# Optimization experiments

Measured on AMD Instinct MI355X. Metric: run time of the kernel, lower is better.

The kernel has to match this reference:

```python
import jax, jax.numpy as jnp
import numpy as np

B, T, C = 2, 2048, 1024
N_HEAD = 16
HEAD_DIM = C // N_HEAD


def setup_inputs() -> dict:
    key = jax.random.key(0)
    k1, k2, k3 = jax.random.split(key, 3)
    x = jax.random.normal(k1, (B, T, C), dtype=jnp.float32)
    # weights stored as [in, out]; torch Linear computes x @ W.T with weight [out, in]
    W_qkv = jax.random.normal(k2, (C, 3 * C), dtype=jnp.float32) * (1.0 / np.sqrt(C))
    W_proj = jax.random.normal(k3, (C, C), dtype=jnp.float32) * (1.0 / np.sqrt(C))
    return {"x": x, "W_qkv": W_qkv, "W_proj": W_proj}


def reference(x, W_qkv, W_proj):
    Bb, Tt, Cc = x.shape
    qkv = x @ W_qkv                                # [B,T,3C]
    q, k, v = jnp.split(qkv, 3, axis=2)
    # [B,T,H,D] -> [B,H,T,D]
    q = q.reshape(Bb, Tt, N_HEAD, HEAD_DIM).transpose(0, 2, 1, 3)
    k = k.reshape(Bb, Tt, N_HEAD, HEAD_DIM).transpose(0, 2, 1, 3)
    v = v.reshape(Bb, Tt, N_HEAD, HEAD_DIM).transpose(0, 2, 1, 3)
    scale = 1.0 / np.sqrt(HEAD_DIM).astype(np.float32)
    att = jnp.einsum('bhqd,bhkd->bhqk', q, k) * scale   # [B,H,T,T]
    causal = jnp.tril(jnp.ones((Tt, Tt), dtype=bool))
    att = jnp.where(causal[None, None], att, -jnp.inf)
    att = jax.nn.softmax(att, axis=-1)
    y = jnp.einsum('bhqk,bhkd->bhqd', att, v)           # [B,H,T,D]
    y = y.transpose(0, 2, 1, 3).reshape(Bb, Tt, Cc)
    return y @ W_proj
```

## Files before the change

kernel.cpp:

```cpp
#include <hip/hip_runtime.h>
#include <hip/hip_bf16.h>
#include <math.h>


typedef __bf16 bf16_t;
typedef __bf16 bf16x4 __attribute__((ext_vector_type(4)));
typedef __bf16 bf16x8 __attribute__((ext_vector_type(8)));
typedef float  f32x4  __attribute__((ext_vector_type(4)));

#define MFMA16(a, b, c) __builtin_amdgcn_mfma_f32_16x16x32_bf16((a), (b), (c), 0, 0, 0)

#define Bn 2
#define Tn 2048
#define Cn 1024
#define Hn 16
#define Dn 64
#define C3 3072
#define Mn 4096
#define QKW 2048
#define NEG_BIG (-1e30f)
#define SCL2 0.18033688011112042f
#define M2   17.31234049066756f

__device__ __forceinline__ void gload_lds16(const void* g, void* l) {
    __builtin_amdgcn_global_load_lds(
        (const __attribute__((address_space(1))) unsigned int*)g,
        (__attribute__((address_space(3))) unsigned int*)l, 16, 0, 0);
}

__global__ __launch_bounds__(256) void transpose_cvt(const float* __restrict__ in,
                                                     bf16_t* __restrict__ out,
                                                     int K, int N) {
    __shared__ float tile[32][33];
    int n0 = blockIdx.x * 32, k0 = blockIdx.y * 32;
    int tx = threadIdx.x, ty = threadIdx.y;
#pragma unroll
    for (int i = 0; i < 32; i += 8)
        tile[ty + i][tx] = in[(size_t)(k0 + ty + i) * N + n0 + tx];
    __syncthreads();
#pragma unroll
    for (int i = 0; i < 32; i += 8)
        out[(size_t)(n0 + ty + i) * K + k0 + tx] = (bf16_t)tile[tx][ty + i];
}

template <typename AT, typename CT, int MODE>
__global__ __launch_bounds__(256) void gemm_m97(const AT* __restrict__ A, int lda,
                                                const bf16_t* __restrict__ BT,
                                                CT* __restrict__ Cout, int ldc, int Kd,
                                                bf16_t* __restrict__ qk,
                                                bf16_t* __restrict__ vT) {
    constexpr bool AF32 = (sizeof(AT) == 4);
    __shared__ AT     As[128 * 32];
    __shared__ bf16_t Bs[128 * 32];

    const int tid = threadIdx.x;
    const int w = tid >> 6, lane = tid & 63;
    const int l16 = lane & 15, quad = lane >> 4;
    const int wm = w & 1, wn = w >> 1;
    const int n0 = blockIdx.x * 128;
    const int m0 = blockIdx.y * 128;

    f32x4 zero = {0.f, 0.f, 0.f, 0.f};
    f32x4 acc[4][4];
#pragma unroll
    for (int mb = 0; mb < 4; mb++)
#pragma unroll
        for (int nb = 0; nb < 4; nb++) acc[mb][nb] = zero;

    for (int k = 0; k < Kd; k += 32) {
        __syncthreads();
        if (AF32) {
#pragma unroll
            for (int j = 0; j < 4; j++) {
                int seg = w * 4 + j;
                int r = seg * 8 + (lane >> 3);
                int cc = (lane & 7) ^ (r & 7);
                const float* g = (const float*)A + (size_t)(m0 + r) * lda + k + cc * 4;
                gload_lds16(g, (char*)As + seg * 1024);
            }
        } else {
#pragma unroll
            for (int j = 0; j < 2; j++) {
                int seg = w * 2 + j;
                int r = seg * 16 + (lane >> 2);
                int cc = (lane & 3) ^ (r & 3);
                const bf16_t* g = (const bf16_t*)A + (size_t)(m0 + r) * lda + k + cc * 8;
                gload_lds16(g, (char*)As + seg * 1024);
            }
        }
#pragma unroll
        for (int j = 0; j < 2; j++) {
            int seg = w * 2 + j;
            int r = seg * 16 + (lane >> 2);
            int cc = (lane & 3) ^ (r & 3);
            const bf16_t* g = BT + (size_t)(n0 + r) * Kd + k + cc * 8;
            gload_lds16(g, (char*)Bs + seg * 1024);
        }
        __syncthreads();

        bf16x8 af[4], bf[4];
#pragma unroll
        for (int mb = 0; mb < 4; mb++) {
            int r = wm * 64 + mb * 16 + l16;
            if (AF32) {
                f32x4 x0 = *(const f32x4*)((const char*)As + (r * 8 + ((quad * 2) ^ (r & 7))) * 16);
                f32x4 x1 = *(const f32x4*)((const char*)As + (r * 8 + ((quad * 2 + 1) ^ (r & 7))) * 16);
                bf16x8 t;
                t[0] = (bf16_t)x0[0]; t[1] = (bf16_t)x0[1]; t[2] = (bf16_t)x0[2]; t[3] = (bf16_t)x0[3];
                t[4] = (bf16_t)x1[0]; t[5] = (bf16_t)x1[1]; t[6] = (bf16_t)x1[2]; t[7] = (bf16_t)x1[3];
                af[mb] = t;
            } else {
                af[mb] = *(const bf16x8*)((const char*)As + (r * 4 + (quad ^ (r & 3))) * 16);
            }
        }
#pragma unroll
        for (int nb = 0; nb < 4; nb++) {
            int r = wn * 64 + nb * 16 + l16;
            bf[nb] = *(const bf16x8*)((const char*)Bs + (r * 4 + (quad ^ (r & 3))) * 16);
        }
#pragma unroll
        for (int mb = 0; mb < 4; mb++)
#pragma unroll
            for (int nb = 0; nb < 4; nb++)
                acc[mb][nb] = MFMA16(af[mb], bf[nb], acc[mb][nb]);
    }

#pragma unroll
    for (int mb = 0; mb < 4; mb++)
#pragma unroll
        for (int nb = 0; nb < 4; nb++) {
            const int col = n0 + wn * 64 + nb * 16 + l16;
            const int row0 = m0 + wm * 64 + mb * 16 + quad * 4;
            if (MODE == 0) {
#pragma unroll
                for (int rr = 0; rr < 4; rr++)
                    Cout[(size_t)(row0 + rr) * ldc + col] = (CT)acc[mb][nb][rr];
            } else {
                if (col < 2048) {
#pragma unroll
                    for (int rr = 0; rr < 4; rr++)
                        qk[(size_t)(row0 + rr) * QKW + col] = (bf16_t)acc[mb][nb][rr];
                } else {
                    int hcol = col - 2048;
                    int bb = row0 >> 11, t0 = row0 & 2047;
                    bf16x4 pv;
#pragma unroll
                    for (int rr = 0; rr < 4; rr++) pv[rr] = (bf16_t)acc[mb][nb][rr];
                    *(bf16x4*)(vT + ((size_t)(bb * 1024 + hcol)) * Tn + t0) = pv;
                }
            }
        }
}

__global__ __launch_bounds__(256) void attn_kernel(bf16_t* __restrict__ qk,
                                                   const bf16_t* __restrict__ vT) {
    const int id = blockIdx.x;
    const int round = id >> 8;
    const int p = id & 255;
    const int bh = p & 31;
    const int xx = p >> 5;
    const int qt = round ? (15 - xx) : xx;
    const int b = bh >> 4, h = bh & 15;

    const int tid = threadIdx.x;
    const int wave = tid >> 6, lane = tid & 63;
    const int l16 = lane & 15, quad = lane >> 4;

    __shared__ bf16_t Kt[64][72];
    __shared__ bf16_t Vt[64][72];
    __shared__ bf16_t Pl[4][32][72];

    bf16_t* qbase = qk + (size_t)b * Tn * QKW + h * Dn;
    const bf16_t* kbase = qk + (size_t)b * Tn * QKW + Cn + h * Dn;
    const bf16_t* vbase = vT + (size_t)(b * 1024 + h * Dn) * Tn;

    const int q0 = qt * 128 + wave * 32;

    bf16x8 qf[2][2];
#pragma unroll
    for (int mb = 0; mb < 2; mb++)
#pragma unroll
        for (int ks = 0; ks < 2; ks++)
            qf[mb][ks] = *(const bf16x8*)(qbase + (size_t)(q0 + mb * 16 + l16) * QKW + ks * 32 + quad * 8);

    bf16x8 ones;
#pragma unroll
    for (int j = 0; j < 8; j++) ones[j] = (bf16_t)1.0f;

    f32x4 zero = {0.f, 0.f, 0.f, 0.f};
    f32x4 o[2][4];
    f32x4 ol[2];
#pragma unroll
    for (int mb = 0; mb < 2; mb++) {
#pragma unroll
        for (int i = 0; i < 4; i++) o[mb][i] = zero;
        ol[mb] = zero;
    }

    const int kbmax = 2 * qt + 1;
    const int kb_mask = 2 * qt + (wave >> 1);

    for (int kb = 0; kb <= kbmax; kb++) {
        __syncthreads();
        const int key0 = kb * 64;
        for (int c = tid; c < 512; c += 256) {
            int r = c >> 3, col = (c & 7) * 8;
            *(bf16x8*)(&Kt[r][col]) = *(const bf16x8*)(kbase + (size_t)(key0 + r) * QKW + col);
            *(bf16x8*)(&Vt[r][col]) = *(const bf16x8*)(vbase + (size_t)r * Tn + key0 + col);
        }
        __syncthreads();

        if (kb <= kb_mask) {
            f32x4 s[2][4];
#pragma unroll
            for (int mb = 0; mb < 2; mb++)
#pragma unroll
                for (int nbk = 0; nbk < 4; nbk++) s[mb][nbk] = zero;
#pragma unroll
            for (int nbk = 0; nbk < 4; nbk++) {
                bf16x8 kf0 = *(const bf16x8*)(&Kt[nbk * 16 + l16][quad * 8]);
                bf16x8 kf1 = *(const bf16x8*)(&Kt[nbk * 16 + l16][32 + quad * 8]);
#pragma unroll
                for (int mb = 0; mb < 2; mb++) {
                    s[mb][nbk] = MFMA16(kf0, qf[mb][0], s[mb][nbk]);
                    s[mb][nbk] = MFMA16(kf1, qf[mb][1], s[mb][nbk]);
                }
            }

            if (kb == kb_mask) {
#pragma unroll
                for (int nbk = 0; nbk < 4; nbk++) {
#pragma unroll
                    for (int mb = 0; mb < 2; mb++) {
                        int q = q0 + mb * 16 + l16;
#pragma unroll
                        for (int r = 0; r < 4; r++) {
                            int key = key0 + nbk * 16 + quad * 4 + r;
                            if (key > q) s[mb][nbk][r] = NEG_BIG;
                        }
                    }
                }
            }

#pragma unroll
            for (int mb = 0; mb < 2; mb++)
#pragma unroll
                for (int nbk = 0; nbk < 4; nbk++) {
                    bf16x4 pk;
#pragma unroll
                    for (int r = 0; r < 4; r++)
                        pk[r] = (bf16_t)__builtin_exp2f(__builtin_fmaf(s[mb][nbk][r], SCL2, -M2));
                    *(bf16x4*)(&Pl[wave][mb * 16 + l16][nbk * 16 + quad * 4]) = pk;
                }

#pragma unroll
            for (int ks = 0; ks < 2; ks++) {
                bf16x8 pf0 = *(const bf16x8*)(&Pl[wave][l16][ks * 32 + quad * 8]);
                bf16x8 pf1 = *(const bf16x8*)(&Pl[wave][16 + l16][ks * 32 + quad * 8]);
#pragma unroll
                for (int nbd = 0; nbd < 4; nbd++) {
                    bf16x8 vf = *(const bf16x8*)(&Vt[nbd * 16 + l16][ks * 32 + quad * 8]);
                    o[0][nbd] = MFMA16(pf0, vf, o[0][nbd]);
                    o[1][nbd] = MFMA16(pf1, vf, o[1][nbd]);
                }
                ol[0] = MFMA16(pf0, ones, ol[0]);
                ol[1] = MFMA16(pf1, ones, ol[1]);
            }
        }
    }

#pragma unroll
    for (int mb = 0; mb < 2; mb++)
#pragma unroll
        for (int nbd = 0; nbd < 4; nbd++)
#pragma unroll
            for (int r = 0; r < 4; r++) {
                int t = q0 + mb * 16 + quad * 4 + r;
                float val = o[mb][nbd][r] / ol[mb][r];
                qbase[(size_t)t * QKW + nbd * 16 + l16] = (bf16_t)val;
            }
}

extern "C" void kernel_launch(void* const* d_in, const int* in_sizes, int n_in,
                              void* d_out, int out_size, void* d_ws, size_t ws_size,
                              hipStream_t stream) {
    const float* x     = (const float*)d_in[0];
    const float* Wqkv  = (const float*)d_in[1];
    const float* Wproj = (const float*)d_in[2];
    float* out = (float*)d_out;

    bf16_t* qk     = (bf16_t*)d_ws;
    bf16_t* vT     = qk + (size_t)Mn * QKW;
    bf16_t* wqkvT  = vT + (size_t)QKW * Tn;
    bf16_t* wprojT = wqkvT + (size_t)C3 * Cn;

    transpose_cvt<<<dim3(C3 / 32, Cn / 32), dim3(32, 8), 0, stream>>>(Wqkv, wqkvT, Cn, C3);
    transpose_cvt<<<dim3(Cn / 32, Cn / 32), dim3(32, 8), 0, stream>>>(Wproj, wprojT, Cn, Cn);

    gemm_m97<float, bf16_t, 1><<<dim3(C3 / 128, Mn / 128), 256, 0, stream>>>(
        x, Cn, wqkvT, (bf16_t*)nullptr, 0, Cn, qk, vT);
    attn_kernel<<<dim3(512), 256, 0, stream>>>(qk, vT);
    gemm_m97<bf16_t, float, 0><<<dim3(Cn / 128, Mn / 128), 256, 0, stream>>>(
        qk, QKW, wprojT, out, Cn, Cn, nullptr, nullptr);
}
```

Before: 213.7 us.

## Halve attention query tile, pre-convert x to bf16, add smaller-tile projection GEMM

The attention kernel now gives each block 64 queries (16 per wave) instead of 128 and launches 1024 blocks, paired so causal work is balanced. This drops the per-wave masked-skip logic and raises parallelism, but K/V tiles are reloaded more often. The input x is converted to bf16 in a separate kernel when workspace allows, so the QKV GEMM reads bf16 instead of fp32. The output projection uses a new 64x128-tile GEMM to get more blocks for the small N=1024 problem.

After: 198.0 us. 1.08x faster.

```diff
diff --git a/kernel.cpp b/kernel.cpp
--- a/kernel.cpp
+++ b/kernel.cpp
@@ -43,6 +43,17 @@
         out[(size_t)(n0 + ty + i) * K + k0 + tx] = (bf16_t)tile[tx][ty + i];
 }
 
+__global__ __launch_bounds__(256) void cvt_bf16(const float* __restrict__ in,
+                                                bf16_t* __restrict__ out) {
+    size_t i = ((size_t)blockIdx.x * 256 + threadIdx.x) * 8;
+    f32x4 a = *(const f32x4*)(in + i);
+    f32x4 b = *(const f32x4*)(in + i + 4);
+    bf16x8 r;
+    r[0] = (bf16_t)a[0]; r[1] = (bf16_t)a[1]; r[2] = (bf16_t)a[2]; r[3] = (bf16_t)a[3];
+    r[4] = (bf16_t)b[0]; r[5] = (bf16_t)b[1]; r[6] = (bf16_t)b[2]; r[7] = (bf16_t)b[3];
+    *(bf16x8*)(out + i) = r;
+}
+
 template <typename AT, typename CT, int MODE>
 __global__ __launch_bounds__(256) void gemm_m97(const AT* __restrict__ A, int lda,
                                                 const bf16_t* __restrict__ BT,
@@ -152,14 +163,81 @@
         }
 }
 
+__global__ __launch_bounds__(256) void gemm_s(const bf16_t* __restrict__ A, int lda,
+                                              const bf16_t* __restrict__ BT,
+                                              float* __restrict__ Cout, int ldc, int Kd) {
+    __shared__ bf16_t As[64 * 32];
+    __shared__ bf16_t Bs[128 * 32];
+
+    const int tid = threadIdx.x;
+    const int w = tid >> 6, lane = tid & 63;
+    const int l16 = lane & 15, quad = lane >> 4;
+    const int wm = w & 1, wn = w >> 1;
+    const int n0 = blockIdx.x * 128;
+    const int m0 = blockIdx.y * 64;
+
+    f32x4 zero = {0.f, 0.f, 0.f, 0.f};
+    f32x4 acc[2][4];
+#pragma unroll
+    for (int mb = 0; mb < 2; mb++)
+#pragma unroll
+        for (int nb = 0; nb < 4; nb++) acc[mb][nb] = zero;
+
+    for (int k = 0; k < Kd; k += 32) {
+        __syncthreads();
+        {
+            int r = w * 16 + (lane >> 2);
+            int cc = (lane & 3) ^ (r & 3);
+            const bf16_t* g = A + (size_t)(m0 + r) * lda + k + cc * 8;
+            gload_lds16(g, (char*)As + w * 1024);
+        }
+#pragma unroll
+        for (int j = 0; j < 2; j++) {
+            int seg = w * 2 + j;
+            int r = seg * 16 + (lane >> 2);
+            int cc = (lane & 3) ^ (r & 3);
+            const bf16_t* g = BT + (size_t)(n0 + r) * Kd + k + cc * 8;
+            gload_lds16(g, (char*)Bs + seg * 1024);
+        }
+        __syncthreads();
+
+        bf16x8 af[2], bf[4];
+#pragma unroll
+        for (int mb = 0; mb < 2; mb++) {
+            int r = wm * 32 + mb * 16 + l16;
+            af[mb] = *(const bf16x8*)((const char*)As + (r * 4 + (quad ^ (r & 3))) * 16);
+        }
+#pragma unroll
+        for (int nb = 0; nb < 4; nb++) {
+            int r = wn * 64 + nb * 16 + l16;
+            bf[nb] = *(const bf16x8*)((const char*)Bs + (r * 4 + (quad ^ (r & 3))) * 16);
+        }
+#pragma unroll
+        for (int mb = 0; mb < 2; mb++)
+#pragma unroll
+            for (int nb = 0; nb < 4; nb++)
+                acc[mb][nb] = MFMA16(af[mb], bf[nb], acc[mb][nb]);
+    }
+
+#pragma unroll
+    for (int mb = 0; mb < 2; mb++)
+#pragma unroll
+        for (int nb = 0; nb < 4; nb++) {
+            const int col = n0 + wn * 64 + nb * 16 + l16;
+            const int row0 = m0 + wm * 32 + mb * 16 + quad * 4;
+#pragma unroll
+            for (int rr = 0; rr < 4; rr++)
+                Cout[(size_t)(row0 + rr) * ldc + col] = acc[mb][nb][rr];
+        }
+}
+
 __global__ __launch_bounds__(256) void attn_kernel(bf16_t* __restrict__ qk,
                                                    const bf16_t* __restrict__ vT) {
     const int id = blockIdx.x;
-    const int round = id >> 8;
-    const int p = id & 255;
-    const int bh = p & 31;
-    const int xx = p >> 5;
-    const int qt = round ? (15 - xx) : xx;
+    const int pair = id >> 1;
+    const int bh = pair & 31;
+    const int xx = pair >> 5;
+    const int qt = (id & 1) ? (31 - xx) : xx;
     const int b = bh >> 4, h = bh & 15;
 
     const int tid = threadIdx.x;
@@ -168,39 +246,31 @@
 
     __shared__ bf16_t Kt[64][72];
     __shared__ bf16_t Vt[64][72];
-    __shared__ bf16_t Pl[4][32][72];
+    __shared__ bf16_t Pl[4][16][72];
 
     bf16_t* qbase = qk + (size_t)b * Tn * QKW + h * Dn;
     const bf16_t* kbase = qk + (size_t)b * Tn * QKW + Cn + h * Dn;
     const bf16_t* vbase = vT + (size_t)(b * 1024 + h * Dn) * Tn;
 
-    const int q0 = qt * 128 + wave * 32;
-
-    bf16x8 qf[2][2];
-#pragma unroll
-    for (int mb = 0; mb < 2; mb++)
-#pragma unroll
-        for (int ks = 0; ks < 2; ks++)
-            qf[mb][ks] = *(const bf16x8*)(qbase + (size_t)(q0 + mb * 16 + l16) * QKW + ks * 32 + quad * 8);
+    const int q0 = qt * 64 + wave * 16;
+
+    bf16x8 qf[2];
+#pragma unroll
+    for (int ks = 0; ks < 2; ks++)
+        qf[ks] = *(const bf16x8*)(qbase + (size_t)(q0 + l16) * QKW + ks * 32 + quad * 8);
 
     bf16x8 ones;
 #pragma unroll
     for (int j = 0; j < 8; j++) ones[j] = (bf16_t)1.0f;
 
     f32x4 zero = {0.f, 0.f, 0.f, 0.f};
-    f32x4 o[2][4];
-    f32x4 ol[2];
-#pragma unroll
-    for (int mb = 0; mb < 2; mb++) {
-#pragma unroll
-        for (int i = 0; i < 4; i++) o[mb][i] = zero;
-        ol[mb] = zero;
-    }
-
-    const int kbmax = 2 * qt + 1;
-    const int kb_mask = 2 * qt + (wave >> 1);
-
-    for (int kb = 0; kb <= kbmax; kb++) {
+    f32x4 o[4];
+    f32x4 ol;
+#pragma unroll
+    for (int i = 0; i < 4; i++) o[i] = zero;
+    ol = zero;
+
+    for (int kb = 0; kb <= qt; kb++) {
         __syncthreads();
         const int key0 = kb * 64;
         for (int c = tid; c < 512; c += 256) {
@@ -210,75 +280,57 @@
         }
         __syncthreads();
 
-        if (kb <= kb_mask) {
-            f32x4 s[2][4];
-#pragma unroll
-            for (int mb = 0; mb < 2; mb++)
-#pragma unroll
-                for (int nbk = 0; nbk < 4; nbk++) s[mb][nbk] = zero;
-#pragma unroll
-            for (int nbk = 0; nbk < 4; nbk++) {
-                bf16x8 kf0 = *(const bf16x8*)(&Kt[nbk * 16 + l16][quad * 8]);
-                bf16x8 kf1 = *(const bf16x8*)(&Kt[nbk * 16 + l16][32 + quad * 8]);
-#pragma unroll
-                for (int mb = 0; mb < 2; mb++) {
-                    s[mb][nbk] = MFMA16(kf0, qf[mb][0], s[mb][nbk]);
-                    s[mb][nbk] = MFMA16(kf1, qf[mb][1], s[mb][nbk]);
+        f32x4 s[4];
+#pragma unroll
+        for (int nbk = 0; nbk < 4; nbk++) s[nbk] = zero;
+#pragma unroll
+        for (int nbk = 0; nbk < 4; nbk++) {
+            bf16x8 kf0 = *(const bf16x8*)(&Kt[nbk * 16 + l16][quad * 8]);
+            bf16x8 kf1 = *(const bf16x8*)(&Kt[nbk * 16 + l16][32 + quad * 8]);
+            s[nbk] = MFMA16(kf0, qf[0], s[nbk]);
+            s[nbk] = MFMA16(kf1, qf[1], s[nbk]);
+        }
+
+        if (kb == qt) {
+            int q = q0 + l16;
+#pragma unroll
+            for (int nbk = 0; nbk < 4; nbk++)
+#pragma unroll
+                for (int r = 0; r < 4; r++) {
+                    int key = key0 + nbk * 16 + quad * 4 + r;
+                    if (key > q) s[nbk][r] = NEG_BIG;
                 }
-            }
-
-            if (kb == kb_mask) {
-#pragma unroll
-                for (int nbk = 0; nbk < 4; nbk++) {
-#pragma unroll
-                    for (int mb = 0; mb < 2; mb++) {
-                        int q = q0 + mb * 16 + l16;
-#pragma unroll
-                        for (int r = 0; r < 4; r++) {
-                            int key = key0 + nbk * 16 + quad * 4 + r;
-                            if (key > q) s[mb][nbk][r] = NEG_BIG;
-                        }
-                    }
-                }
-            }
-
-#pragma unroll
-            for (int mb = 0; mb < 2; mb++)
-#pragma unroll
-                for (int nbk = 0; nbk < 4; nbk++) {
-                    bf16x4 pk;
-#pragma unroll
-                    for (int r = 0; r < 4; r++)
-                        pk[r] = (bf16_t)__builtin_exp2f(__builtin_fmaf(s[mb][nbk][r], SCL2, -M2));
-                    *(bf16x4*)(&Pl[wave][mb * 16 + l16][nbk * 16 + quad * 4]) = pk;
-                }
-
-#pragma unroll
-            for (int ks = 0; ks < 2; ks++) {
-                bf16x8 pf0 = *(const bf16x8*)(&Pl[wave][l16][ks * 32 + quad * 8]);
-                bf16x8 pf1 = *(const bf16x8*)(&Pl[wave][16 + l16][ks * 32 + quad * 8]);
-#pragma unroll
-                for (int nbd = 0; nbd < 4; nbd++) {
-                    bf16x8 vf = *(const bf16x8*)(&Vt[nbd * 16 + l16][ks * 32 + quad * 8]);
-                    o[0][nbd] = MFMA16(pf0, vf, o[0][nbd]);
-                    o[1][nbd] = MFMA16(pf1, vf, o[1][nbd]);
-                }
-                ol[0] = MFMA16(pf0, ones, ol[0]);
-                ol[1] = MFMA16(pf1, ones, ol[1]);
-            }
+        }
+
+#pragma unroll
+        for (int nbk = 0; nbk < 4; nbk++) {
+            bf16x4 pk;
+#pragma unroll
+            for (int r = 0; r < 4; r++)
+                pk[r] = (bf16_t)__builtin_exp2f(__builtin_fmaf(s[nbk][r], SCL2, -M2));
+            *(bf16x4*)(&Pl[wave][l16][nbk * 16 + quad * 4]) = pk;
+        }
+
+#pragma unroll
+        for (int ks = 0; ks < 2; ks++) {
+            bf16x8 pf = *(const bf16x8*)(&Pl[wave][l16][ks * 32 + quad * 8]);
+#pragma unroll
+            for (int nbd = 0; nbd < 4; nbd++) {
+                bf16x8 vf = *(const bf16x8*)(&Vt[nbd * 16 + l16][ks * 32 + quad * 8]);
+                o[nbd] = MFMA16(pf, vf, o[nbd]);
+            }
+            ol = MFMA16(pf, ones, ol);
         }
     }
 
 #pragma unroll
-    for (int mb = 0; mb < 2; mb++)
-#pragma unroll
-        for (int nbd = 0; nbd < 4; nbd++)
-#pragma unroll
-            for (int r = 0; r < 4; r++) {
-                int t = q0 + mb * 16 + quad * 4 + r;
-                float val = o[mb][nbd][r] / ol[mb][r];
-                qbase[(size_t)t * QKW + nbd * 16 + l16] = (bf16_t)val;
-            }
+    for (int nbd = 0; nbd < 4; nbd++)
+#pragma unroll
+        for (int r = 0; r < 4; r++) {
+            int t = q0 + quad * 4 + r;
+            float val = o[nbd][r] / ol[r];
+            qbase[(size_t)t * QKW + nbd * 16 + l16] = (bf16_t)val;
+        }
 }
 
 extern "C" void kernel_launch(void* const* d_in, const int* in_sizes, int n_in,
@@ -293,13 +345,22 @@
     bf16_t* vT     = qk + (size_t)Mn * QKW;
     bf16_t* wqkvT  = vT + (size_t)QKW * Tn;
     bf16_t* wprojT = wqkvT + (size_t)C3 * Cn;
+    bf16_t* xb     = wprojT + (size_t)Cn * Cn;
+
+    const size_t NEED_XB = ((size_t)Mn * QKW + (size_t)QKW * Tn + (size_t)C3 * Cn +
+                            (size_t)Cn * Cn + (size_t)Mn * Cn) * sizeof(bf16_t);
 
     transpose_cvt<<<dim3(C3 / 32, Cn / 32), dim3(32, 8), 0, stream>>>(Wqkv, wqkvT, Cn, C3);
     transpose_cvt<<<dim3(Cn / 32, Cn / 32), dim3(32, 8), 0, stream>>>(Wproj, wprojT, Cn, Cn);
 
-    gemm_m97<float, bf16_t, 1><<<dim3(C3 / 128, Mn / 128), 256, 0, stream>>>(
-        x, Cn, wqkvT, (bf16_t*)nullptr, 0, Cn, qk, vT);
-    attn_kernel<<<dim3(512), 256, 0, stream>>>(qk, vT);
-    gemm_m97<bf16_t, float, 0><<<dim3(Cn / 128, Mn / 128), 256, 0, stream>>>(
-        qk, QKW, wprojT, out, Cn, Cn, nullptr, nullptr);
-}
+    if (ws_size >= NEED_XB) {
+        cvt_bf16<<<dim3((Mn * Cn) / 2048), 256, 0, stream>>>(x, xb);
+        gemm_m97<bf16_t, bf16_t, 1><<<dim3(C3 / 128, Mn / 128), 256, 0, stream>>>(
+            xb, Cn, wqkvT, (bf16_t*)nullptr, 0, Cn, qk, vT);
+    } else {
+        gemm_m97<float, bf16_t, 1><<<dim3(C3 / 128, Mn / 128), 256, 0, stream>>>(
+            x, Cn, wqkvT, (bf16_t*)nullptr, 0, Cn, qk, vT);
+    }
+    attn_kernel<<<dim3(1024), 256, 0, stream>>>(qk, vT);
+    gemm_s<<<dim3(Cn / 128, Mn / 64), 256, 0, stream>>>(qk, QKW, wprojT, out, Cn, Cn);
+}
```
